# Optimization experiments

Hardware: AMD Instinct MI355X
Metric: run time of the kernel (lower is better)

Reference implementation:

```python
import jax, jax.numpy as jnp
import numpy as np

B, E, D = 4096, 64, 1024

def setup_inputs() -> dict:
    key = jax.random.key(0)
    k1, k2 = jax.random.split(key)
    z = jax.random.normal(k1, (B, D), dtype=jnp.float32)
    expert_keys = jax.random.normal(k2, (E, D), dtype=jnp.float32)
    log_sigma = jnp.zeros((D,), dtype=jnp.float32)
    return {"z": z, "expert_keys": expert_keys, "log_sigma": log_sigma}

def reference(z, expert_keys, log_sigma):
    # diag(sigma_inv) @ diff followed by (. * diff).sum(-1) is exactly an
    # elementwise-scaled squared distance: sum_d exp(-log_sigma_d) * diff_d^2
    sigma_inv = jnp.exp(-log_sigma)                              # [D]
    diff = z[:, None, :] - expert_keys[None, :, :]               # [B, E, D]
    mahalanobis_dist = jnp.einsum('bed,d,bed->be', diff, sigma_inv, diff)  # [B, E]
    similarity = 1.0 / (1.0 + mahalanobis_dist)                  # [B, E]
    weights = jax.nn.softmax(similarity, axis=-1)                # [B, E]
    weighted_expert = weights @ expert_keys                      # [B, D]
    return (similarity, weighted_expert)
```

## Files before the change

### kernel.cpp

```cpp
#include <hip/hip_runtime.h>
#include <hip/hip_bf16.h>

#define B_N 4096
#define E_N 64
#define D_N 1024
#define ROWS 16

typedef __bf16 bf16x8 __attribute__((ext_vector_type(8)));
typedef __bf16 bf16x4 __attribute__((ext_vector_type(4)));
typedef float f32x4 __attribute__((ext_vector_type(4)));


__global__ __launch_bounds__(256) void prep_kernel(
    const float* __restrict__ keys, const float* __restrict__ lsig,
    float* __restrict__ sinv, float* __restrict__ ak,
    __bf16* __restrict__ sk, __bf16* __restrict__ kT)
{
  __shared__ float red[4];
  __shared__ __bf16 tl[64][72];
  const int bid = blockIdx.x;
  const int t = threadIdx.x;

  if (bid < 64) {
    const int e = bid;
    const float4 k4 = *(const float4*)(keys + e * D_N + 4 * t);
    const float4 l4 = *(const float4*)(lsig + 4 * t);
    float4 s4;
    s4.x = expf(-l4.x); s4.y = expf(-l4.y); s4.z = expf(-l4.z); s4.w = expf(-l4.w);
    if (e == 0) *(float4*)(sinv + 4 * t) = s4;
    const float4 sk4 = make_float4(s4.x * k4.x, s4.y * k4.y, s4.z * k4.z, s4.w * k4.w);
    bf16x4 skb;
    skb[0] = (__bf16)sk4.x; skb[1] = (__bf16)sk4.y; skb[2] = (__bf16)sk4.z; skb[3] = (__bf16)sk4.w;
    *(bf16x4*)(sk + e * D_N + 4 * t) = skb;
    float p = sk4.x * k4.x + sk4.y * k4.y + sk4.z * k4.z + sk4.w * k4.w;
    #pragma unroll
    for (int off = 32; off > 0; off >>= 1) p += __shfl_down(p, off);
    if ((t & 63) == 0) red[t >> 6] = p;
    __syncthreads();
    if (t == 0) ak[e] = red[0] + red[1] + red[2] + red[3];
  } else {
    const int d0 = (bid - 64) * 64;
    #pragma unroll
    for (int p = 0; p < 4; ++p) {
      const int e  = p * 16 + (t >> 4);
      const int dd = (t & 15) * 4;
      const float4 k4 = *(const float4*)(keys + (size_t)e * D_N + d0 + dd);
      tl[dd + 0][e] = (__bf16)k4.x; tl[dd + 1][e] = (__bf16)k4.y;
      tl[dd + 2][e] = (__bf16)k4.z; tl[dd + 3][e] = (__bf16)k4.w;
    }
    __syncthreads();
    #pragma unroll
    for (int p = 0; p < 2; ++p) {
      const int dd = p * 32 + (t >> 3);
      const int l8 = t & 7;
      const bf16x8 v = *(const bf16x8*)&tl[dd][l8 * 8];
      *(bf16x8*)(kT + (size_t)(d0 + dd) * E_N + l8 * 8) = v;
    }
  }
}

__global__ __launch_bounds__(256) void main_kernel(
    const float* __restrict__ z, const float* __restrict__ sinv,
    const float* __restrict__ ak, const __bf16* __restrict__ sk,
    const __bf16* __restrict__ kT,
    float* __restrict__ out_sim, float* __restrict__ out_we)
{
  constexpr int ZS = D_N + 8;
  __shared__ __bf16 zlds[ROWS * ZS];
  __shared__ float azs[ROWS];
  __shared__ float simb[ROWS][68];
  __shared__ __bf16 wlds[ROWS][72];

  const int t  = threadIdx.x;
  const int b0 = blockIdx.x * ROWS;

  const int sr = t >> 4;
  const int sc = t & 15;
  const float* zrow = z + (size_t)(b0 + sr) * D_N;
  float az = 0.f;
  #pragma unroll
  for (int l = 0; l < 16; ++l) {
    const int c = sc * 4 + l * 64;
    const float4 z4 = *(const float4*)(zrow + c);
    const float4 s4 = *(const float4*)(sinv + c);
    az += s4.x * z4.x * z4.x + s4.y * z4.y * z4.y + s4.z * z4.z * z4.z + s4.w * z4.w * z4.w;
    bf16x4 zb;
    zb[0] = (__bf16)z4.x; zb[1] = (__bf16)z4.y; zb[2] = (__bf16)z4.z; zb[3] = (__bf16)z4.w;
    *(bf16x4*)(&zlds[sr * ZS + c]) = zb;
  }
  az += __shfl_xor(az, 1); az += __shfl_xor(az, 2);
  az += __shfl_xor(az, 4); az += __shfl_xor(az, 8);
  if (sc == 0) azs[sr] = az;
  __syncthreads();

  const int wave = t >> 6;
  const int lane = t & 63;
  const int ln = lane & 15;
  const int q  = lane >> 4;

  const float akv = ak[wave * 16 + ln];
  f32x4 acc = {0.f, 0.f, 0.f, 0.f};
  const __bf16* bp = sk + (size_t)(wave * 16 + ln) * D_N + q * 8;
  const __bf16* ap = &zlds[ln * ZS + q * 8];
  #pragma unroll 8
  for (int ks = 0; ks < 32; ++ks) {
    const bf16x8 bfr = *(const bf16x8*)(bp + ks * 32);
    const bf16x8 afr = *(const bf16x8*)(ap + ks * 32);
    acc = __builtin_amdgcn_mfma_f32_16x16x32_bf16(afr, bfr, acc, 0, 0, 0);
  }

  #pragma unroll
  for (int i = 0; i < 4; ++i) {
    const int row = q * 4 + i;
    const float dist = azs[row] + akv - 2.0f * acc[i];
    simb[row][wave * 16 + ln] = 1.0f / (1.0f + dist);
  }

  const __bf16* kp0 = kT + (size_t)(wave * 16 + ln) * E_N + q * 8;
  const bf16x8 pb0 = *(const bf16x8*)(kp0);
  const bf16x8 pb1 = *(const bf16x8*)(kp0 + 32);

  __syncthreads();

  if (t < 64) {
    const int row = t >> 2, seg = t & 3;
    float v[16];
    #pragma unroll
    for (int i = 0; i < 16; ++i) v[i] = simb[row][seg * 16 + i];
    float mx = v[0];
    #pragma unroll
    for (int i = 1; i < 16; ++i) mx = fmaxf(mx, v[i]);
    mx = fmaxf(mx, __shfl_xor(mx, 1));
    mx = fmaxf(mx, __shfl_xor(mx, 2));
    float sum = 0.f;
    #pragma unroll
    for (int i = 0; i < 16; ++i) { v[i] = __expf(v[i] - mx); sum += v[i]; }
    sum += __shfl_xor(sum, 1);
    sum += __shfl_xor(sum, 2);
    const float inv = 1.0f / sum;
    #pragma unroll
    for (int i = 0; i < 16; ++i) wlds[row][seg * 16 + i] = (__bf16)(v[i] * inv);
  }
  __syncthreads();

  {
    const float4 sv = *(const float4*)&simb[t >> 4][(t & 15) * 4];
    *(float4*)(out_sim + (size_t)(b0 + (t >> 4)) * E_N + (t & 15) * 4) = sv;
  }

  const bf16x8 a0 = *(const bf16x8*)&wlds[ln][q * 8];
  const bf16x8 a1 = *(const bf16x8*)&wlds[ln][32 + q * 8];
  #pragma unroll
  for (int i = 0; i < 16; ++i) {
    const int dt = wave + 4 * i;
    const int d0 = dt * 16;
    bf16x8 b0f, b1f;
    if (i == 0) { b0f = pb0; b1f = pb1; }
    else {
      const __bf16* kp = kT + (size_t)(d0 + ln) * E_N + q * 8;
      b0f = *(const bf16x8*)(kp);
      b1f = *(const bf16x8*)(kp + 32);
    }
    f32x4 o = {0.f, 0.f, 0.f, 0.f};
    o = __builtin_amdgcn_mfma_f32_16x16x32_bf16(a0, b0f, o, 0, 0, 0);
    o = __builtin_amdgcn_mfma_f32_16x16x32_bf16(a1, b1f, o, 0, 0, 0);
    #pragma unroll
    for (int j = 0; j < 4; ++j)
      out_we[(size_t)(b0 + q * 4 + j) * D_N + d0 + ln] = o[j];
  }
}

extern "C" void kernel_launch(void* const* d_in, const int* in_sizes, int n_in,
                              void* d_out, int out_size, void* d_ws, size_t ws_size,
                              hipStream_t stream)
{
  const float* z    = (const float*)d_in[0];
  const float* keys = (const float*)d_in[1];
  const float* ls   = (const float*)d_in[2];
  float* out_sim = (float*)d_out;
  float* out_we  = out_sim + (size_t)B_N * E_N;
  char* ws = (char*)d_ws;
  float*  sinv = (float*)(ws);
  float*  ak   = (float*)(ws + 4096);
  __bf16* sk   = (__bf16*)(ws + 4352);
  __bf16* kT   = (__bf16*)(ws + 135424);
  prep_kernel<<<80, 256, 0, stream>>>(keys, ls, sinv, ak, sk, kT);
  main_kernel<<<B_N / ROWS, 256, 0, stream>>>(z, sinv, ak, sk, kT, out_sim, out_we);
}
```

Before: 83.55 us.

## Overlap z staging with first-half MFMA, parallelize softmax, vectorize output stores

Splits the z load and bf16 conversion into halves so the first half of the distance MFMA loop runs while the second half of z is still being fetched and converted. Softmax now runs across all four waves, with 16 lanes per row and shuffle reductions, instead of a single wave. The weighted-expert MFMA swaps its operands so each lane holds four consecutive output columns and writes them with one 16-byte store instead of four scalar strided stores. It adds an extra barrier and raises register pressure from the buffered z values.

```diff
diff --git a/kernel.cpp b/kernel.cpp
--- a/kernel.cpp
+++ b/kernel.cpp
@@ -73,13 +73,17 @@
 
   const int t  = threadIdx.x;
   const int b0 = blockIdx.x * ROWS;
+  const int wave = t >> 6;
+  const int lane = t & 63;
+  const int ln = lane & 15;
+  const int q  = lane >> 4;
 
   const int sr = t >> 4;
   const int sc = t & 15;
   const float* zrow = z + (size_t)(b0 + sr) * D_N;
   float az = 0.f;
   #pragma unroll
-  for (int l = 0; l < 16; ++l) {
+  for (int l = 0; l < 8; ++l) {
     const int c = sc * 4 + l * 64;
     const float4 z4 = *(const float4*)(zrow + c);
     const float4 s4 = *(const float4*)(sinv + c);
@@ -88,58 +92,84 @@
     zb[0] = (__bf16)z4.x; zb[1] = (__bf16)z4.y; zb[2] = (__bf16)z4.z; zb[3] = (__bf16)z4.w;
     *(bf16x4*)(&zlds[sr * ZS + c]) = zb;
   }
+  const float akv = ak[wave * 16 + ln];
+  __syncthreads();
+
+  f32x4 acc = {0.f, 0.f, 0.f, 0.f};
+  const __bf16* bp = sk + (size_t)(wave * 16 + ln) * D_N + q * 8;
+  const __bf16* ap = &zlds[ln * ZS + q * 8];
+  {
+    float4 z4b[4], s4b[4];
+    #pragma unroll
+    for (int l = 0; l < 4; ++l) {
+      const int c = 512 + sc * 4 + l * 64;
+      z4b[l] = *(const float4*)(zrow + c);
+      s4b[l] = *(const float4*)(sinv + c);
+    }
+    #pragma unroll
+    for (int ks = 0; ks < 16; ++ks) {
+      const bf16x8 bfr = *(const bf16x8*)(bp + ks * 32);
+      const bf16x8 afr = *(const bf16x8*)(ap + ks * 32);
+      acc = __builtin_amdgcn_mfma_f32_16x16x32_bf16(afr, bfr, acc, 0, 0, 0);
+    }
+    #pragma unroll
+    for (int l = 0; l < 4; ++l) {
+      const int c = 512 + sc * 4 + l * 64;
+      const float4 z4 = z4b[l], s4 = s4b[l];
+      az += s4.x * z4.x * z4.x + s4.y * z4.y * z4.y + s4.z * z4.z * z4.z + s4.w * z4.w * z4.w;
+      bf16x4 zb;
+      zb[0] = (__bf16)z4.x; zb[1] = (__bf16)z4.y; zb[2] = (__bf16)z4.z; zb[3] = (__bf16)z4.w;
+      *(bf16x4*)(&zlds[sr * ZS + c]) = zb;
+    }
+    #pragma unroll
+    for (int l = 0; l < 4; ++l) {
+      const int c = 768 + sc * 4 + l * 64;
+      const float4 z4 = *(const float4*)(zrow + c);
+      const float4 s4 = *(const float4*)(sinv + c);
+      az += s4.x * z4.x * z4.x + s4.y * z4.y * z4.y + s4.z * z4.z * z4.z + s4.w * z4.w * z4.w;
+      bf16x4 zb;
+      zb[0] = (__bf16)z4.x; zb[1] = (__bf16)z4.y; zb[2] = (__bf16)z4.z; zb[3] = (__bf16)z4.w;
+      *(bf16x4*)(&zlds[sr * ZS + c]) = zb;
+    }
+  }
   az += __shfl_xor(az, 1); az += __shfl_xor(az, 2);
   az += __shfl_xor(az, 4); az += __shfl_xor(az, 8);
   if (sc == 0) azs[sr] = az;
   __syncthreads();
 
-  const int wave = t >> 6;
-  const int lane = t & 63;
-  const int ln = lane & 15;
-  const int q  = lane >> 4;
-
-  const float akv = ak[wave * 16 + ln];
-  f32x4 acc = {0.f, 0.f, 0.f, 0.f};
-  const __bf16* bp = sk + (size_t)(wave * 16 + ln) * D_N + q * 8;
-  const __bf16* ap = &zlds[ln * ZS + q * 8];
-  #pragma unroll 8
-  for (int ks = 0; ks < 32; ++ks) {
+  #pragma unroll
+  for (int ks = 16; ks < 32; ++ks) {
     const bf16x8 bfr = *(const bf16x8*)(bp + ks * 32);
     const bf16x8 afr = *(const bf16x8*)(ap + ks * 32);
     acc = __builtin_amdgcn_mfma_f32_16x16x32_bf16(afr, bfr, acc, 0, 0, 0);
   }
-
   #pragma unroll
   for (int i = 0; i < 4; ++i) {
     const int row = q * 4 + i;
     const float dist = azs[row] + akv - 2.0f * acc[i];
     simb[row][wave * 16 + ln] = 1.0f / (1.0f + dist);
   }
-
-  const __bf16* kp0 = kT + (size_t)(wave * 16 + ln) * E_N + q * 8;
-  const bf16x8 pb0 = *(const bf16x8*)(kp0);
-  const bf16x8 pb1 = *(const bf16x8*)(kp0 + 32);
-
-  __syncthreads();
-
-  if (t < 64) {
-    const int row = t >> 2, seg = t & 3;
-    float v[16];
-    #pragma unroll
-    for (int i = 0; i < 16; ++i) v[i] = simb[row][seg * 16 + i];
-    float mx = v[0];
-    #pragma unroll
-    for (int i = 1; i < 16; ++i) mx = fmaxf(mx, v[i]);
-    mx = fmaxf(mx, __shfl_xor(mx, 1));
-    mx = fmaxf(mx, __shfl_xor(mx, 2));
-    float sum = 0.f;
-    #pragma unroll
-    for (int i = 0; i < 16; ++i) { v[i] = __expf(v[i] - mx); sum += v[i]; }
-    sum += __shfl_xor(sum, 1);
-    sum += __shfl_xor(sum, 2);
+  const __bf16* kp0 = kT + (size_t)(wave * 256 + ln) * E_N + q * 8;
+  const bf16x8 pa0 = *(const bf16x8*)(kp0);
+  const bf16x8 pa1 = *(const bf16x8*)(kp0 + 32);
+  __syncthreads();
+
+  {
+    const int row = wave * 4 + q;
+    const f32x4 v4 = *(const f32x4*)&simb[row][ln * 4];
+    float mx = fmaxf(fmaxf(v4[0], v4[1]), fmaxf(v4[2], v4[3]));
+    mx = fmaxf(mx, __shfl_xor(mx, 1)); mx = fmaxf(mx, __shfl_xor(mx, 2));
+    mx = fmaxf(mx, __shfl_xor(mx, 4)); mx = fmaxf(mx, __shfl_xor(mx, 8));
+    float e0 = __expf(v4[0] - mx), e1 = __expf(v4[1] - mx);
+    float e2 = __expf(v4[2] - mx), e3 = __expf(v4[3] - mx);
+    float sum = e0 + e1 + e2 + e3;
+    sum += __shfl_xor(sum, 1); sum += __shfl_xor(sum, 2);
+    sum += __shfl_xor(sum, 4); sum += __shfl_xor(sum, 8);
     const float inv = 1.0f / sum;
-    #pragma unroll
-    for (int i = 0; i < 16; ++i) wlds[row][seg * 16 + i] = (__bf16)(v[i] * inv);
+    bf16x4 wv;
+    wv[0] = (__bf16)(e0 * inv); wv[1] = (__bf16)(e1 * inv);
+    wv[2] = (__bf16)(e2 * inv); wv[3] = (__bf16)(e3 * inv);
+    *(bf16x4*)&wlds[row][ln * 4] = wv;
   }
   __syncthreads();
 
@@ -148,25 +178,23 @@
     *(float4*)(out_sim + (size_t)(b0 + (t >> 4)) * E_N + (t & 15) * 4) = sv;
   }
 
-  const bf16x8 a0 = *(const bf16x8*)&wlds[ln][q * 8];
-  const bf16x8 a1 = *(const bf16x8*)&wlds[ln][32 + q * 8];
+  const bf16x8 wb0 = *(const bf16x8*)&wlds[ln][q * 8];
+  const bf16x8 wb1 = *(const bf16x8*)&wlds[ln][32 + q * 8];
+  float* orow = out_we + (size_t)(b0 + ln) * D_N + wave * 256 + q * 4;
   #pragma unroll
   for (int i = 0; i < 16; ++i) {
-    const int dt = wave + 4 * i;
-    const int d0 = dt * 16;
-    bf16x8 b0f, b1f;
-    if (i == 0) { b0f = pb0; b1f = pb1; }
+    const int d0 = wave * 256 + i * 16;
+    bf16x8 a0f, a1f;
+    if (i == 0) { a0f = pa0; a1f = pa1; }
     else {
       const __bf16* kp = kT + (size_t)(d0 + ln) * E_N + q * 8;
-      b0f = *(const bf16x8*)(kp);
-      b1f = *(const bf16x8*)(kp + 32);
+      a0f = *(const bf16x8*)(kp);
+      a1f = *(const bf16x8*)(kp + 32);
     }
     f32x4 o = {0.f, 0.f, 0.f, 0.f};
-    o = __builtin_amdgcn_mfma_f32_16x16x32_bf16(a0, b0f, o, 0, 0, 0);
-    o = __builtin_amdgcn_mfma_f32_16x16x32_bf16(a1, b1f, o, 0, 0, 0);
-    #pragma unroll
-    for (int j = 0; j < 4; ++j)
-      out_we[(size_t)(b0 + q * 4 + j) * D_N + d0 + ln] = o[j];
+    o = __builtin_amdgcn_mfma_f32_16x16x32_bf16(a0f, wb0, o, 0, 0, 0);
+    o = __builtin_amdgcn_mfma_f32_16x16x32_bf16(a1f, wb1, o, 0, 0, 0);
+    *(f32x4*)(orow + i * 16) = o;
   }
 }
 
```

Measured after the change: 86.79 us. +3.9%, slower.
